# Kernel optimization log

Measured on AMD Instinct MI355X. Metric: run time of the kernel, lower is better.

## Reference

```python
import jax, jax.numpy as jnp
import numpy as np

N = 50000
IN_CH = 128
HID = 256
HEADS = 8
HEAD_DIM = HID // HEADS
NUM_CLASSES = 2
E = 800000
NEG_SLOPE = 0.2  # PyG GATConv default leaky_relu slope


def gat_conv(x, edge_index, W, att_src, att_dst, bias):
    """PyG-style GATConv (concat=True, add_self_loops=True, eval mode).
    x: [N, HID]; edge_index: [2, E] (row 0 = source j, row 1 = target i).
    W: [HID, HEADS*HEAD_DIM]; att_src/att_dst: [HEADS, HEAD_DIM]; bias: [HEADS*HEAD_DIM].
    """
    loop = jnp.arange(N)
    src = jnp.concatenate([edge_index[0], loop])  # self-loops appended
    dst = jnp.concatenate([edge_index[1], loop])
    h = (x @ W).reshape(N, HEADS, HEAD_DIM)          # [N, H, D]
    a_src = jnp.einsum('nhd,hd->nh', h, att_src)     # [N, H]
    a_dst = jnp.einsum('nhd,hd->nh', h, att_dst)
    e = jax.nn.leaky_relu(a_src[src] + a_dst[dst], NEG_SLOPE)  # [E+N, H]
    # segment softmax over incoming edges of each target node
    m = jax.ops.segment_max(e, dst, num_segments=N)
    p = jnp.exp(e - m[dst])
    s = jax.ops.segment_sum(p, dst, num_segments=N)
    alpha = p / (s[dst] + 1e-16)                     # [E+N, H]
    msg = h[src] * alpha[:, :, None]                 # [E+N, H, D]
    out = jax.ops.segment_sum(msg, dst, num_segments=N)  # [N, H, D]
    return out.reshape(N, HEADS * HEAD_DIM) + bias


def setup_inputs() -> dict:
    key = jax.random.key(0)
    ks = jax.random.split(key, 24)
    g = lambda k, shape, fan_in: jax.random.normal(k, shape, dtype=jnp.float32) / np.sqrt(fan_in)
    inp = {}
    inp['x'] = jax.random.normal(ks[0], (N, IN_CH), dtype=jnp.float32)
    inp['tut_edge_index'] = jax.random.randint(ks[1], (2, E), 0, N)
    inp['tdt_edge_index'] = jax.random.randint(ks[2], (2, E), 0, N)
    inp['proj_W'] = g(ks[3], (IN_CH, HID), IN_CH)
    inp['proj_b'] = jnp.zeros((HID,), jnp.float32)
    # 2 GAT layers per meta-path, stacked on leading axis
    inp['tut_W'] = g(ks[4], (2, HID, HID), HID)
    inp['tut_asrc'] = g(ks[5], (2, HEADS, HEAD_DIM), HEAD_DIM)
    inp['tut_adst'] = g(ks[6], (2, HEADS, HEAD_DIM), HEAD_DIM)
    inp['tut_bias'] = jnp.zeros((2, HID), jnp.float32)
    inp['tdt_W'] = g(ks[7], (2, HID, HID), HID)
    inp['tdt_asrc'] = g(ks[8], (2, HEADS, HEAD_DIM), HEAD_DIM)
    inp['tdt_adst'] = g(ks[9], (2, HEADS, HEAD_DIM), HEAD_DIM)
    inp['tdt_bias'] = jnp.zeros((2, HID), jnp.float32)
    inp['sem_att'] = jnp.full((2,), 0.5, jnp.float32)
    inp['cls_W1'] = g(ks[10], (HID, HID // 2), HID)
    inp['cls_b1'] = jnp.zeros((HID // 2,), jnp.float32)
    inp['cls_W2'] = g(ks[11], (HID // 2, NUM_CLASSES), HID // 2)
    inp['cls_b2'] = jnp.zeros((NUM_CLASSES,), jnp.float32)
    return inp


def reference(x, tut_edge_index, tdt_edge_index, proj_W, proj_b,
              tut_W, tut_asrc, tut_adst, tut_bias,
              tdt_W, tdt_asrc, tdt_adst, tdt_bias,
              sem_att, cls_W1, cls_b1, cls_W2, cls_b2):
    h = x @ proj_W + proj_b
    # TUT branch: 2 GATConv layers (eval mode -> dropout is identity)
    h_tut = h
    for l in range(2):
        h_tut = gat_conv(h_tut, tut_edge_index, tut_W[l], tut_asrc[l], tut_adst[l], tut_bias[l])
        h_tut = jax.nn.elu(h_tut)
    # TDT branch
    h_tdt = h
    for l in range(2):
        h_tdt = gat_conv(h_tdt, tdt_edge_index, tdt_W[l], tdt_asrc[l], tdt_adst[l], tdt_bias[l])
        h_tdt = jax.nn.elu(h_tdt)
    w = jax.nn.softmax(sem_att)
    z = w[0] * h_tut + w[1] * h_tdt
    hc = jax.nn.relu(z @ cls_W1 + cls_b1)
    logits = hc @ cls_W2 + cls_b2  # [N, NUM_CLASSES]
    return logits
```

## Files before the change

kernel.cpp:

```cpp
#include <hip/hip_runtime.h>
#include <hip/hip_fp16.h>
#include <cstddef>
#include <cstdint>


#define HID        256
#define HEADS      8
#define NEG_SLOPE  0.2f

#define BSH     7
#define BNODES  128
#define MAXNB   512
#define CH      2048

typedef __attribute__((ext_vector_type(8))) short short8v;
typedef __attribute__((ext_vector_type(4))) float float4v;

static __device__ __forceinline__ unsigned short f32_to_bf16(float v) {
    union { float f; unsigned u; } c; c.f = v;
    unsigned r = c.u + 0x7FFFu + ((c.u >> 16) & 1u);
    return (unsigned short)(r >> 16);
}
static __device__ __forceinline__ float bf16_to_f32(unsigned short b) {
    union { unsigned u; float f; } c; c.u = ((unsigned)b) << 16;
    return c.f;
}
static __device__ __forceinline__ void split_bf16(float v, unsigned short& hi, unsigned short& lo) {
    hi = f32_to_bf16(v);
    lo = f32_to_bf16(v - bf16_to_f32(hi));
}
static __device__ __forceinline__ void gload_lds16(const void* g, void* l) {
    __builtin_amdgcn_global_load_lds((const __attribute__((address_space(1))) void*)g,
                                     (__attribute__((address_space(3))) void*)l, 16, 0, 0);
}

template<int MODE>
__global__ __launch_bounds__(256) void mfma_gemm_kernel(
    const unsigned short* __restrict__ Ahi, const unsigned short* __restrict__ Alo,
    const unsigned short* __restrict__ Bthi, const unsigned short* __restrict__ Btlo,
    const float* __restrict__ bias,
    unsigned short* __restrict__ Chi, unsigned short* __restrict__ Clo,
    __half* __restrict__ Cf16, float* __restrict__ Cf32,
    int M, int N, int K)
{
    __shared__ __align__(16) short lds[4 * 4096];

    const int tid  = threadIdx.x;
    const int lane = tid & 63;
    const int w    = tid >> 6;
    const int wr   = w >> 1;
    const int wc   = w & 1;
    const int m0   = blockIdx.y * 128;
    const int n0   = blockIdx.x * 128;

    const unsigned short* sbase = (w == 0) ? Ahi : (w == 1) ? Alo : (w == 2) ? Bthi : Btlo;
    const int rowbase = (w < 2) ? m0 : n0;
    const int rowlim  = ((w < 2) ? M : N) - 1;

    float4v acc[4][4];
    #pragma unroll
    for (int i = 0; i < 4; ++i)
        #pragma unroll
        for (int j = 0; j < 4; ++j)
            acc[i][j] = (float4v){0.f, 0.f, 0.f, 0.f};

    const int kcl = lane >> 4;
    const int rl  = lane & 15;

    for (int k0 = 0; k0 < K; k0 += 32) {
        #pragma unroll
        for (int rh = 0; rh < 2; ++rh) {
            int row = rowbase + rh * 64 + lane;
            row = row > rowlim ? rowlim : row;
            const unsigned short* src = sbase + (size_t)row * K + k0;
            #pragma unroll
            for (int kc = 0; kc < 4; ++kc) {
                short* dst = &lds[w * 4096 + kc * 1024 + rh * 512];
                gload_lds16(src + kc * 8, dst);
            }
        }
        __syncthreads();

        short8v ahi[4], alo[4], bhi[4], blo[4];
        #pragma unroll
        for (int i = 0; i < 4; ++i) {
            int am = wr * 64 + i * 16 + rl;
            int bn = wc * 64 + i * 16 + rl;
            ahi[i] = *(const short8v*)&lds[0 * 4096 + kcl * 1024 + am * 8];
            alo[i] = *(const short8v*)&lds[1 * 4096 + kcl * 1024 + am * 8];
            bhi[i] = *(const short8v*)&lds[2 * 4096 + kcl * 1024 + bn * 8];
            blo[i] = *(const short8v*)&lds[3 * 4096 + kcl * 1024 + bn * 8];
        }
        #pragma unroll
        for (int i = 0; i < 4; ++i)
            #pragma unroll
            for (int j = 0; j < 4; ++j) {
                acc[i][j] = __builtin_amdgcn_mfma_f32_16x16x32_bf16(ahi[i], bhi[j], acc[i][j], 0, 0, 0);
                acc[i][j] = __builtin_amdgcn_mfma_f32_16x16x32_bf16(ahi[i], blo[j], acc[i][j], 0, 0, 0);
                acc[i][j] = __builtin_amdgcn_mfma_f32_16x16x32_bf16(alo[i], bhi[j], acc[i][j], 0, 0, 0);
            }
        __syncthreads();
    }

    const int cr = (lane >> 4) * 4;
    #pragma unroll
    for (int i = 0; i < 4; ++i) {
        #pragma unroll
        for (int r = 0; r < 4; ++r) {
            int row = m0 + wr * 64 + i * 16 + cr + r;
            if (row >= M) continue;
            #pragma unroll
            for (int j = 0; j < 4; ++j) {
                int col = n0 + wc * 64 + j * 16 + rl;
                float v = acc[i][j][r];
                if (bias) v += bias[col];
                if (MODE == 0) {
                    unsigned short h, l;
                    split_bf16(v, h, l);
                    Chi[(size_t)row * N + col] = h;
                    Clo[(size_t)row * N + col] = l;
                } else if (MODE == 1) {
                    Cf16[(size_t)row * N + col] = __float2half(v);
                } else {
                    Cf32[(size_t)row * N + col] = fmaxf(v, 0.f);
                }
            }
        }
    }
}

__global__ void prep_kernel(
    const float* __restrict__ proj_W, const float* __restrict__ tut_W,
    const float* __restrict__ tdt_W, const float* __restrict__ cls_W1,
    unsigned short* __restrict__ pWthi, unsigned short* __restrict__ pWtlo,
    unsigned short* __restrict__ tWthi, unsigned short* __restrict__ tWtlo,
    unsigned short* __restrict__ dWthi, unsigned short* __restrict__ dWtlo,
    unsigned short* __restrict__ cWthi, unsigned short* __restrict__ cWtlo,
    const float* __restrict__ x,
    unsigned short* __restrict__ xhi, unsigned short* __restrict__ xlo, int count4x)
{
    const int tid = blockIdx.x * blockDim.x + threadIdx.x;
    const int stride = gridDim.x * blockDim.x;
    for (int idx = tid; idx < 327680; idx += stride) {
        unsigned short h, l;
        if (idx < 32768) {
            int k = idx >> 8, n = idx & 255;
            split_bf16(proj_W[idx], h, l);
            pWthi[n * 128 + k] = h; pWtlo[n * 128 + k] = l;
        } else if (idx < 163840) {
            int r = idx - 32768;
            int ly = r >> 16, rr = r & 65535;
            int k = rr >> 8, n = rr & 255;
            split_bf16(tut_W[r], h, l);
            tWthi[ly * 65536 + n * 256 + k] = h; tWtlo[ly * 65536 + n * 256 + k] = l;
        } else if (idx < 294912) {
            int r = idx - 163840;
            int ly = r >> 16, rr = r & 65535;
            int k = rr >> 8, n = rr & 255;
            split_bf16(tdt_W[r], h, l);
            dWthi[ly * 65536 + n * 256 + k] = h; dWtlo[ly * 65536 + n * 256 + k] = l;
        } else {
            int r = idx - 294912;
            int k = r >> 7, n = r & 127;
            split_bf16(cls_W1[r], h, l);
            cWthi[n * 256 + k] = h; cWtlo[n * 256 + k] = l;
        }
    }
    for (int i = tid; i < count4x; i += stride) {
        float4 v = reinterpret_cast<const float4*>(x)[i];
        ushort4 hh, ll;
        split_bf16(v.x, hh.x, ll.x);
        split_bf16(v.y, hh.y, ll.y);
        split_bf16(v.z, hh.z, ll.z);
        split_bf16(v.w, hh.w, ll.w);
        reinterpret_cast<ushort4*>(xhi)[i] = hh;
        reinterpret_cast<ushort4*>(xlo)[i] = ll;
    }
}

__global__ __launch_bounds__(256) void att_kernel(
    const __half* __restrict__ hW,
    const float* __restrict__ att_src, const float* __restrict__ att_dst,
    float* __restrict__ a_src, float* __restrict__ a_dst, int n_nodes)
{
    const int wave = threadIdx.x >> 6;
    const int lane = threadIdx.x & 63;
    const int n = blockIdx.x * 4 + wave;
    if (n >= n_nodes) return;

    const __half2* hp = reinterpret_cast<const __half2*>(&hW[(size_t)n * HID + lane * 4]);
    __half2 h01 = hp[0], h23 = hp[1];
    float hx = __low2float(h01), hy = __high2float(h01);
    float hz = __low2float(h23), hw = __high2float(h23);
    float4 s4 = *reinterpret_cast<const float4*>(&att_src[lane * 4]);
    float4 d4 = *reinterpret_cast<const float4*>(&att_dst[lane * 4]);
    float ps = hx * s4.x + hy * s4.y + hz * s4.z + hw * s4.w;
    float pd = hx * d4.x + hy * d4.y + hz * d4.z + hw * d4.w;
    #pragma unroll
    for (int off = 1; off < 8; off <<= 1) {
        ps += __shfl_xor(ps, off);
        pd += __shfl_xor(pd, off);
    }
    if ((lane & 7) == 0) {
        a_src[n * HEADS + (lane >> 3)] = ps;
        a_dst[n * HEADS + (lane >> 3)] = pd;
    }
}

template<int OMODE>
__global__ __launch_bounds__(256) void gat_kernel(
    const __half* __restrict__ hW,
    const float* __restrict__ a_src, const float* __restrict__ a_dst,
    const int* __restrict__ row_ptr, const int* __restrict__ adj,
    const float* __restrict__ bias,
    const unsigned short* __restrict__ prevHi, const unsigned short* __restrict__ prevLo,
    const float* __restrict__ sem,
    unsigned short* __restrict__ outhi, unsigned short* __restrict__ outlo,
    int n_nodes)
{
    const int wave = threadIdx.x >> 6;
    const int lane = threadIdx.x & 63;
    const int n = blockIdx.x * 4 + wave;
    if (n >= n_nodes) return;

    const int beg = row_ptr[n];
    const int end = row_ptr[n + 1];
    const int h2 = lane >> 3;
    const int sl = lane & 7;
    const int lane4 = lane * 4;
    const int gbase = lane & 56;

    const float adst = a_dst[n * HEADS + h2];

    float m = -INFINITY, s = 0.f;
    float4 acc = make_float4(0.f, 0.f, 0.f, 0.f);

    for (int j = beg; j < end; j += 8) {
        const int js = j + sl;
        const int valid = js < end;
        int src_l = valid ? adj[js] : 0;
        float e = -INFINITY;
        if (valid) {
            e = a_src[src_l * HEADS + h2] + adst;
            e = (e > 0.f) ? e : NEG_SLOPE * e;
        }
        float me = e;
        me = fmaxf(me, __shfl_xor(me, 1));
        me = fmaxf(me, __shfl_xor(me, 2));
        me = fmaxf(me, __shfl_xor(me, 4));
        const float m_new = fmaxf(m, me);
        const float scale = __expf(m - m_new);
        const float p = __expf(e - m_new);
        float ps = p;
        ps += __shfl_xor(ps, 1);
        ps += __shfl_xor(ps, 2);
        ps += __shfl_xor(ps, 4);
        s = s * scale + ps;
        m = m_new;
        acc.x *= scale; acc.y *= scale; acc.z *= scale; acc.w *= scale;

        #pragma unroll
        for (int jj = 0; jj < 8; ++jj) {
            if (j + jj >= end) break;
            const float alpha = __shfl(p, gbase | jj);
            const int src = __shfl(src_l, jj);
            const __half2* hp = reinterpret_cast<const __half2*>(&hW[(size_t)src * HID + lane4]);
            __half2 v01 = hp[0], v23 = hp[1];
            acc.x += alpha * __low2float(v01);
            acc.y += alpha * __high2float(v01);
            acc.z += alpha * __low2float(v23);
            acc.w += alpha * __high2float(v23);
        }
    }

    const float inv = 1.f / (s + 1e-16f);
    float4 bv = *reinterpret_cast<const float4*>(&bias[lane4]);
    float4 o;
    o.x = acc.x * inv + bv.x; o.y = acc.y * inv + bv.y;
    o.z = acc.z * inv + bv.z; o.w = acc.w * inv + bv.w;
    o.x = (o.x > 0.f) ? o.x : expm1f(o.x);
    o.y = (o.y > 0.f) ? o.y : expm1f(o.y);
    o.z = (o.z > 0.f) ? o.z : expm1f(o.z);
    o.w = (o.w > 0.f) ? o.w : expm1f(o.w);

    if (OMODE == 1) {
        const float e0 = __expf(sem[0]);
        const float e1 = __expf(sem[1]);
        const float w0 = e0 / (e0 + e1);
        const float w1 = e1 / (e0 + e1);
        ushort4 ph = *reinterpret_cast<const ushort4*>(&prevHi[(size_t)n * HID + lane4]);
        ushort4 pl = *reinterpret_cast<const ushort4*>(&prevLo[(size_t)n * HID + lane4]);
        o.x = w0 * (bf16_to_f32(ph.x) + bf16_to_f32(pl.x)) + w1 * o.x;
        o.y = w0 * (bf16_to_f32(ph.y) + bf16_to_f32(pl.y)) + w1 * o.y;
        o.z = w0 * (bf16_to_f32(ph.z) + bf16_to_f32(pl.z)) + w1 * o.z;
        o.w = w0 * (bf16_to_f32(ph.w) + bf16_to_f32(pl.w)) + w1 * o.w;
    }

    ushort4 oh, ol;
    split_bf16(o.x, oh.x, ol.x);
    split_bf16(o.y, oh.y, ol.y);
    split_bf16(o.z, oh.z, ol.z);
    split_bf16(o.w, oh.w, ol.w);
    *reinterpret_cast<ushort4*>(&outhi[(size_t)n * HID + lane4]) = oh;
    *reinterpret_cast<ushort4*>(&outlo[(size_t)n * HID + lane4]) = ol;
}

__global__ __launch_bounds__(256) void bucket_count_kernel(
    const int* __restrict__ tut_dst, const int* __restrict__ tdt_dst,
    int* __restrict__ gcount, int E, int NB)
{
    __shared__ int hist[MAXNB];
    const int g = blockIdx.y;
    const int* dstp = g ? tdt_dst : tut_dst;
    for (int i = threadIdx.x; i < MAXNB; i += 256) hist[i] = 0;
    __syncthreads();
    for (int e = blockIdx.x * 256 + threadIdx.x; e < E; e += gridDim.x * 256)
        atomicAdd(&hist[dstp[e] >> BSH], 1);
    __syncthreads();
    for (int i = threadIdx.x; i < NB; i += 256) {
        int c = hist[i];
        if (c) atomicAdd(&gcount[g * NB + i], c);
    }
}

__global__ __launch_bounds__(512) void bucket_scan_kernel(
    const int* __restrict__ gcount, int* __restrict__ ebase, int* __restrict__ adjbase,
    int* __restrict__ rp0, int* __restrict__ rp1, int N, int E, int NB)
{
    __shared__ int sa[MAXNB], sb[MAXNB];
    const int t = threadIdx.x;
    for (int g = 0; g < 2; ++g) {
        int cnt = (t < NB) ? gcount[g * NB + t] : 0;
        int nodes = 0;
        if (t < NB) { int s = t << BSH; nodes = (N - s < BNODES) ? (N - s) : BNODES; }
        sa[t] = cnt;
        sb[t] = cnt + nodes;
        __syncthreads();
        for (int off = 1; off < MAXNB; off <<= 1) {
            int va = (t >= off) ? sa[t - off] : 0;
            int vb = (t >= off) ? sb[t - off] : 0;
            __syncthreads();
            sa[t] += va; sb[t] += vb;
            __syncthreads();
        }
        if (t < NB) {
            ebase[g * (NB + 1) + t + 1] = sa[t];
            adjbase[g * (NB + 1) + t + 1] = sb[t];
        }
        if (t == 0) { ebase[g * (NB + 1)] = 0; adjbase[g * (NB + 1)] = 0; }
        __syncthreads();
    }
    if (t == 0) { rp0[N] = E + N; rp1[N] = E + N; }
}

__global__ __launch_bounds__(256) void bucket_bin_kernel(
    const int* __restrict__ tut_ei, const int* __restrict__ tdt_ei,
    const int* __restrict__ ebase, int* __restrict__ gcursor,
    int2* __restrict__ ebuf, int E, int NB)
{
    __shared__ int lhist[MAXNB];
    __shared__ int lbase[MAXNB];
    __shared__ int loffs[MAXNB];
    __shared__ int2 spair[CH];
    __shared__ int saddr[CH];
    const int g = blockIdx.y;
    const int* ei = g ? tdt_ei : tut_ei;
    const int e0 = blockIdx.x * CH;
    const int cnt = (E - e0 < CH) ? (E - e0) : CH;

    for (int i = threadIdx.x; i < MAXNB; i += 256) lhist[i] = 0;
    __syncthreads();

    int myb[8], myrank[8], mysrc[8], mydst[8];
    int nmine = 0;
    #pragma unroll
    for (int k = 0; k < 8; ++k) {
        int idx = e0 + threadIdx.x + k * 256;
        if (idx < e0 + cnt) {
            int sv = ei[idx];
            int dv = ei[E + idx];
            int b = dv >> BSH;
            int r = atomicAdd(&lhist[b], 1);
            myb[nmine] = b; myrank[nmine] = r; mysrc[nmine] = sv; mydst[nmine] = dv;
            ++nmine;
        }
    }
    __syncthreads();
    loffs[threadIdx.x] = lhist[threadIdx.x];
    loffs[threadIdx.x + 256] = lhist[threadIdx.x + 256];
    __syncthreads();
    for (int off = 1; off < MAXNB; off <<= 1) {
        int i0 = threadIdx.x, i1 = threadIdx.x + 256;
        int v0 = (i0 >= off) ? loffs[i0 - off] : 0;
        int v1 = (i1 >= off) ? loffs[i1 - off] : 0;
        __syncthreads();
        loffs[i0] += v0; loffs[i1] += v1;
        __syncthreads();
    }
    for (int i = threadIdx.x; i < NB; i += 256) {
        int c = lhist[i];
        lbase[i] = c ? atomicAdd(&gcursor[g * NB + i], c) : 0;
    }
    __syncthreads();
    const int* eb = ebase + g * (NB + 1);
    for (int k = 0; k < nmine; ++k) {
        int b = myb[k];
        int sorted = loffs[b] - lhist[b] + myrank[k];
        spair[sorted] = make_int2(mysrc[k], mydst[k]);
        saddr[sorted] = eb[b] + lbase[b] + myrank[k];
    }
    __syncthreads();
    int2* out = ebuf + (size_t)g * E;
    for (int i = threadIdx.x; i < cnt; i += 256)
        out[saddr[i]] = spair[i];
}

__global__ __launch_bounds__(256) void bucket_csr_kernel(
    const int* __restrict__ gcount, const int* __restrict__ ebase,
    const int* __restrict__ adjbase, const int2* __restrict__ ebuf,
    int* __restrict__ rp0, int* __restrict__ rp1,
    int* __restrict__ adj0, int* __restrict__ adj1, int N, int E, int NB)
{
    __shared__ int hist[BNODES], scn[BNODES], cursor[BNODES];
    const int g = blockIdx.y;
    const int b = blockIdx.x;
    int* rp  = g ? rp1 : rp0;
    int* adj = g ? adj1 : adj0;
    const int cnt = gcount[g * NB + b];
    const int aB  = adjbase[g * (NB + 1) + b];
    const int node0 = b << BSH;
    const int nb = (N - node0 < BNODES) ? (N - node0) : BNODES;
    const int2* ep = ebuf + (size_t)g * E + ebase[g * (NB + 1) + b];
    const int t = threadIdx.x;

    if (t < BNODES) hist[t] = 0;
    __syncthreads();
    for (int e = t; e < cnt; e += 256)
        atomicAdd(&hist[ep[e].y - node0], 1);
    __syncthreads();
    if (t < BNODES) scn[t] = (t < nb) ? hist[t] + 1 : 0;
    __syncthreads();
    for (int off = 1; off < BNODES; off <<= 1) {
        int v = 0;
        if (t < BNODES && t >= off) v = scn[t - off];
        __syncthreads();
        if (t < BNODES) scn[t] += v;
        __syncthreads();
    }
    if (t < nb) {
        int s = scn[t] - hist[t] - 1;
        rp[node0 + t] = aB + s;
        adj[aB + s] = node0 + t;
        cursor[t] = s + 1;
    }
    __syncthreads();
    for (int e = t; e < cnt; e += 256) {
        int2 pr = ep[e];
        int pos = atomicAdd(&cursor[pr.y - node0], 1);
        adj[aB + pos] = pr.x;
    }
}

__global__ __launch_bounds__(256) void cls2_kernel(
    const float* __restrict__ hc, const float* __restrict__ W2,
    const float* __restrict__ b2, float* __restrict__ out, int n_nodes)
{
    const int wave = threadIdx.x >> 6;
    const int lane = threadIdx.x & 63;
    const int n = blockIdx.x * 4 + wave;
    if (n >= n_nodes) return;
    float h0 = hc[(size_t)n * 128 + lane];
    float h1 = hc[(size_t)n * 128 + 64 + lane];
    float p0 = h0 * W2[lane * 2 + 0] + h1 * W2[(64 + lane) * 2 + 0];
    float p1 = h0 * W2[lane * 2 + 1] + h1 * W2[(64 + lane) * 2 + 1];
    #pragma unroll
    for (int off = 1; off < 64; off <<= 1) {
        p0 += __shfl_xor(p0, off);
        p1 += __shfl_xor(p1, off);
    }
    if (lane == 0) {
        out[(size_t)n * 2 + 0] = p0 + b2[0];
        out[(size_t)n * 2 + 1] = p1 + b2[1];
    }
}

extern "C" void kernel_launch(void* const* d_in, const int* in_sizes, int n_in,
                              void* d_out, int out_size, void* d_ws, size_t ws_size,
                              hipStream_t stream)
{
    const float* x        = (const float*)d_in[0];
    const int*   tut_ei   = (const int*)d_in[1];
    const int*   tdt_ei   = (const int*)d_in[2];
    const float* proj_W   = (const float*)d_in[3];
    const float* proj_b   = (const float*)d_in[4];
    const float* tut_W    = (const float*)d_in[5];
    const float* tut_asrc = (const float*)d_in[6];
    const float* tut_adst = (const float*)d_in[7];
    const float* tut_bias = (const float*)d_in[8];
    const float* tdt_W    = (const float*)d_in[9];
    const float* tdt_asrc = (const float*)d_in[10];
    const float* tdt_adst = (const float*)d_in[11];
    const float* tdt_bias = (const float*)d_in[12];
    const float* sem_att  = (const float*)d_in[13];
    const float* cls_W1   = (const float*)d_in[14];
    const float* cls_b1   = (const float*)d_in[15];
    const float* cls_W2   = (const float*)d_in[16];
    const float* cls_b2   = (const float*)d_in[17];

    const int IN_CH = 128;
    const int N = in_sizes[0] / IN_CH;
    const int E = in_sizes[1] / 2;
    const int NB = (N + BNODES - 1) >> BSH;
    const size_t NH = (size_t)N * HID;
    const size_t NI = (size_t)N * IN_CH;

    char* base = (char*)d_ws;
    size_t off = 0;
    auto alloc = [&](size_t bytes) -> void* {
        void* p = base + off;
        off = (off + bytes + 255) & ~(size_t)255;
        return p;
    };
    unsigned short* xhi  = (unsigned short*)alloc(NI * 2);
    unsigned short* xlo  = (unsigned short*)alloc(NI * 2);
    unsigned short* t2lo = (unsigned short*)alloc(NH * 2);
    unsigned short* h0hi = (unsigned short*)alloc(NH * 2);
    unsigned short* h0lo = (unsigned short*)alloc(NH * 2);
    unsigned short* l1hi = (unsigned short*)alloc(NH * 2);
    unsigned short* l1lo = (unsigned short*)alloc(NH * 2);
    __half*         hWf  = (__half*)alloc(NH * 2);
    float* a_src = (float*)alloc((size_t)N * HEADS * sizeof(float));
    float* a_dst = (float*)alloc((size_t)N * HEADS * sizeof(float));
    unsigned short* pWthi = (unsigned short*)alloc(256 * 128 * 2);
    unsigned short* pWtlo = (unsigned short*)alloc(256 * 128 * 2);
    unsigned short* tWthi = (unsigned short*)alloc(2 * 256 * 256 * 2);
    unsigned short* tWtlo = (unsigned short*)alloc(2 * 256 * 256 * 2);
    unsigned short* dWthi = (unsigned short*)alloc(2 * 256 * 256 * 2);
    unsigned short* dWtlo = (unsigned short*)alloc(2 * 256 * 256 * 2);
    unsigned short* cWthi = (unsigned short*)alloc(128 * 256 * 2);
    unsigned short* cWtlo = (unsigned short*)alloc(128 * 256 * 2);
    int* rp_tut  = (int*)alloc((size_t)(N + 1) * sizeof(int));
    int* adj_tut = (int*)alloc((size_t)(E + N) * sizeof(int));
    int* rp_tdt  = (int*)alloc((size_t)(N + 1) * sizeof(int));
    int* adj_tdt = (int*)alloc((size_t)(E + N) * sizeof(int));
    int* gbuf    = (int*)alloc((size_t)4 * NB * sizeof(int));
    int* gcount  = gbuf;
    int* gcursor = gbuf + 2 * NB;
    int* ebase   = (int*)alloc((size_t)2 * (NB + 1) * sizeof(int));
    int* adjbase = (int*)alloc((size_t)2 * (NB + 1) * sizeof(int));
    (void)ws_size; (void)n_in; (void)out_size;

    int2* ebuf = (int2*)hWf;
    unsigned short* t2hi = xhi;
    unsigned short* zhi  = l1hi;
    unsigned short* zlo  = l1lo;
    float*          hc   = (float*)hWf;

    const int nodeBlocks = (N + 3) / 4;

    hipMemsetAsync(gbuf, 0, (size_t)4 * NB * sizeof(int), stream);
    prep_kernel<<<1024, 256, 0, stream>>>(proj_W, tut_W, tdt_W, cls_W1,
                                          pWthi, pWtlo, tWthi, tWtlo, dWthi, dWtlo,
                                          cWthi, cWtlo, x, xhi, xlo, (int)(NI / 4));
    bucket_count_kernel<<<dim3(128, 2), 256, 0, stream>>>(tut_ei + E, tdt_ei + E, gcount, E, NB);
    bucket_scan_kernel<<<1, 512, 0, stream>>>(gcount, ebase, adjbase, rp_tut, rp_tdt, N, E, NB);
    bucket_bin_kernel<<<dim3((E + CH - 1) / CH, 2), 256, 0, stream>>>(
        tut_ei, tdt_ei, ebase, gcursor, ebuf, E, NB);
    bucket_csr_kernel<<<dim3(NB, 2), 256, 0, stream>>>(
        gcount, ebase, adjbase, ebuf, rp_tut, rp_tdt, adj_tut, adj_tdt, N, E, NB);

    const int gy = (N + 127) / 128;

    mfma_gemm_kernel<0><<<dim3(2, gy), 256, 0, stream>>>(
        xhi, xlo, pWthi, pWtlo, proj_b, h0hi, h0lo, nullptr, nullptr, N, HID, IN_CH);

    auto run_gemm_att = [&](const unsigned short* ahi, const unsigned short* alo,
                            const unsigned short* wthi, const unsigned short* wtlo,
                            const float* asrc_w, const float* adst_w) {
        mfma_gemm_kernel<1><<<dim3(2, gy), 256, 0, stream>>>(
            ahi, alo, wthi, wtlo, nullptr, nullptr, nullptr, hWf, nullptr, N, HID, HID);
        att_kernel<<<nodeBlocks, 256, 0, stream>>>(hWf, asrc_w, adst_w, a_src, a_dst, N);
    };

    const int WT = 256 * 256;
    const int AS = HEADS * (HID / HEADS);

    run_gemm_att(h0hi, h0lo, tWthi, tWtlo, tut_asrc, tut_adst);
    gat_kernel<0><<<nodeBlocks, 256, 0, stream>>>(
        hWf, a_src, a_dst, rp_tut, adj_tut, tut_bias,
        nullptr, nullptr, nullptr, l1hi, l1lo, N);
    run_gemm_att(l1hi, l1lo, tWthi + WT, tWtlo + WT, tut_asrc + AS, tut_adst + AS);
    gat_kernel<0><<<nodeBlocks, 256, 0, stream>>>(
        hWf, a_src, a_dst, rp_tut, adj_tut, tut_bias + HID,
        nullptr, nullptr, nullptr, t2hi, t2lo, N);
    run_gemm_att(h0hi, h0lo, dWthi, dWtlo, tdt_asrc, tdt_adst);
    gat_kernel<0><<<nodeBlocks, 256, 0, stream>>>(
        hWf, a_src, a_dst, rp_tdt, adj_tdt, tdt_bias,
        nullptr, nullptr, nullptr, l1hi, l1lo, N);
    run_gemm_att(l1hi, l1lo, dWthi + WT, dWtlo + WT, tdt_asrc + AS, tdt_adst + AS);
    gat_kernel<1><<<nodeBlocks, 256, 0, stream>>>(
        hWf, a_src, a_dst, rp_tdt, adj_tdt, tdt_bias + HID,
        t2hi, t2lo, sem_att, zhi, zlo, N);

    mfma_gemm_kernel<2><<<dim3(1, gy), 256, 0, stream>>>(
        zhi, zlo, cWthi, cWtlo, cls_b1, nullptr, nullptr, nullptr, hc, N, 128, HID);
    cls2_kernel<<<nodeBlocks, 256, 0, stream>>>(hc, cls_W2, cls_b2, (float*)d_out, N);
}
```

Before: 759.3 us.

## Fuse first-layer GEMMs of both branches, two-pass GAT softmax, pack edge pairs

Merges the first GAT layer projection of the TUT and TDT branches into a single 512-wide GEMM sharing the h0 input, writing two separate fp16 outputs. Rewrites the GAT aggregation as a two-pass scheme: first a per-head max/sum reduction across lanes, then an unrolled gather loop with precomputed normalized alphas, which removes the per-chunk rescaling and shuffles. Packs source and local destination into one int in the CSR build to halve edge buffer traffic. The two-pass approach reads adj and a_src twice, and the buffer aliasing is more involved.

```diff
diff --git a/kernel.cpp b/kernel.cpp
--- a/kernel.cpp
+++ b/kernel.cpp
@@ -40,7 +40,7 @@
     const unsigned short* __restrict__ Bthi, const unsigned short* __restrict__ Btlo,
     const float* __restrict__ bias,
     unsigned short* __restrict__ Chi, unsigned short* __restrict__ Clo,
-    __half* __restrict__ Cf16, float* __restrict__ Cf32,
+    __half* __restrict__ Cf16a, __half* __restrict__ Cf16b, float* __restrict__ Cf32,
     int M, int N, int K)
 {
     __shared__ __align__(16) short lds[4 * 4096];
@@ -120,7 +120,8 @@
                     Chi[(size_t)row * N + col] = h;
                     Clo[(size_t)row * N + col] = l;
                 } else if (MODE == 1) {
-                    Cf16[(size_t)row * N + col] = __float2half(v);
+                    if (col < 256) Cf16a[(size_t)row * 256 + col] = __float2half(v);
+                    else           Cf16b[(size_t)row * 256 + (col - 256)] = __float2half(v);
                 } else {
                     Cf32[(size_t)row * N + col] = fmaxf(v, 0.f);
                 }
@@ -133,8 +134,9 @@
     const float* __restrict__ proj_W, const float* __restrict__ tut_W,
     const float* __restrict__ tdt_W, const float* __restrict__ cls_W1,
     unsigned short* __restrict__ pWthi, unsigned short* __restrict__ pWtlo,
-    unsigned short* __restrict__ tWthi, unsigned short* __restrict__ tWtlo,
-    unsigned short* __restrict__ dWthi, unsigned short* __restrict__ dWtlo,
+    unsigned short* __restrict__ w1hi,  unsigned short* __restrict__ w1lo,
+    unsigned short* __restrict__ t2Whi, unsigned short* __restrict__ t2Wlo,
+    unsigned short* __restrict__ d2Whi, unsigned short* __restrict__ d2Wlo,
     unsigned short* __restrict__ cWthi, unsigned short* __restrict__ cWtlo,
     const float* __restrict__ x,
     unsigned short* __restrict__ xhi, unsigned short* __restrict__ xlo, int count4x)
@@ -152,13 +154,15 @@
             int ly = r >> 16, rr = r & 65535;
             int k = rr >> 8, n = rr & 255;
             split_bf16(tut_W[r], h, l);
-            tWthi[ly * 65536 + n * 256 + k] = h; tWtlo[ly * 65536 + n * 256 + k] = l;
+            if (ly == 0) { w1hi[n * 256 + k] = h;  w1lo[n * 256 + k] = l; }
+            else         { t2Whi[n * 256 + k] = h; t2Wlo[n * 256 + k] = l; }
         } else if (idx < 294912) {
             int r = idx - 163840;
             int ly = r >> 16, rr = r & 65535;
             int k = rr >> 8, n = rr & 255;
             split_bf16(tdt_W[r], h, l);
-            dWthi[ly * 65536 + n * 256 + k] = h; dWtlo[ly * 65536 + n * 256 + k] = l;
+            if (ly == 0) { w1hi[(256 + n) * 256 + k] = h; w1lo[(256 + n) * 256 + k] = l; }
+            else         { d2Whi[n * 256 + k] = h;        d2Wlo[n * 256 + k] = l; }
         } else {
             int r = idx - 294912;
             int k = r >> 7, n = r & 127;
@@ -225,59 +229,83 @@
 
     const int beg = row_ptr[n];
     const int end = row_ptr[n + 1];
+    const int h1 = lane & 7;
+    const float adst1 = a_dst[n * HEADS + h1];
+
+    float m = -INFINITY, s = 0.f;
+    for (int j = beg + (lane >> 3); j < end; j += 8) {
+        float e = a_src[adj[j] * HEADS + h1] + adst1;
+        e = (e > 0.f) ? e : NEG_SLOPE * e;
+        float mn = fmaxf(m, e);
+        float t = (m > -INFINITY) ? s * __expf(m - mn) : 0.f;
+        s = t + __expf(e - mn);
+        m = mn;
+    }
+    #pragma unroll
+    for (int off = 8; off < 64; off <<= 1) {
+        float mo = __shfl_xor(m, off);
+        float so = __shfl_xor(s, off);
+        float mn = fmaxf(m, mo);
+        float t1 = (m  > -INFINITY) ? s  * __expf(m  - mn) : 0.f;
+        float t2 = (mo > -INFINITY) ? so * __expf(mo - mn) : 0.f;
+        s = t1 + t2;
+        m = mn;
+    }
+
     const int h2 = lane >> 3;
-    const int sl = lane & 7;
+    const float mh  = __shfl(m, h2);
+    const float sh  = __shfl(s, h2);
+    const float inv = 1.f / (sh + 1e-16f);
+    const float adst2 = a_dst[n * HEADS + h2];
     const int lane4 = lane * 4;
-    const int gbase = lane & 56;
-
-    const float adst = a_dst[n * HEADS + h2];
-
-    float m = -INFINITY, s = 0.f;
+
     float4 acc = make_float4(0.f, 0.f, 0.f, 0.f);
-
-    for (int j = beg; j < end; j += 8) {
-        const int js = j + sl;
-        const int valid = js < end;
-        int src_l = valid ? adj[js] : 0;
-        float e = -INFINITY;
-        if (valid) {
-            e = a_src[src_l * HEADS + h2] + adst;
-            e = (e > 0.f) ? e : NEG_SLOPE * e;
-        }
-        float me = e;
-        me = fmaxf(me, __shfl_xor(me, 1));
-        me = fmaxf(me, __shfl_xor(me, 2));
-        me = fmaxf(me, __shfl_xor(me, 4));
-        const float m_new = fmaxf(m, me);
-        const float scale = __expf(m - m_new);
-        const float p = __expf(e - m_new);
-        float ps = p;
-        ps += __shfl_xor(ps, 1);
-        ps += __shfl_xor(ps, 2);
-        ps += __shfl_xor(ps, 4);
-        s = s * scale + ps;
-        m = m_new;
-        acc.x *= scale; acc.y *= scale; acc.z *= scale; acc.w *= scale;
-
-        #pragma unroll
-        for (int jj = 0; jj < 8; ++jj) {
-            if (j + jj >= end) break;
-            const float alpha = __shfl(p, gbase | jj);
-            const int src = __shfl(src_l, jj);
-            const __half2* hp = reinterpret_cast<const __half2*>(&hW[(size_t)src * HID + lane4]);
-            __half2 v01 = hp[0], v23 = hp[1];
-            acc.x += alpha * __low2float(v01);
-            acc.y += alpha * __high2float(v01);
-            acc.z += alpha * __low2float(v23);
-            acc.w += alpha * __high2float(v23);
-        }
-    }
-
-    const float inv = 1.f / (s + 1e-16f);
+    int j = beg;
+    for (; j + 4 <= end; j += 4) {
+        int s0 = adj[j + 0], s1 = adj[j + 1], s2 = adj[j + 2], s3 = adj[j + 3];
+        float e0 = a_src[s0 * HEADS + h2] + adst2;
+        float e1 = a_src[s1 * HEADS + h2] + adst2;
+        float e2 = a_src[s2 * HEADS + h2] + adst2;
+        float e3 = a_src[s3 * HEADS + h2] + adst2;
+        e0 = (e0 > 0.f) ? e0 : NEG_SLOPE * e0;
+        e1 = (e1 > 0.f) ? e1 : NEG_SLOPE * e1;
+        e2 = (e2 > 0.f) ? e2 : NEG_SLOPE * e2;
+        e3 = (e3 > 0.f) ? e3 : NEG_SLOPE * e3;
+        float al0 = __expf(e0 - mh) * inv;
+        float al1 = __expf(e1 - mh) * inv;
+        float al2 = __expf(e2 - mh) * inv;
+        float al3 = __expf(e3 - mh) * inv;
+        const __half2* p0 = reinterpret_cast<const __half2*>(&hW[(size_t)s0 * HID + lane4]);
+        const __half2* p1 = reinterpret_cast<const __half2*>(&hW[(size_t)s1 * HID + lane4]);
+        const __half2* p2 = reinterpret_cast<const __half2*>(&hW[(size_t)s2 * HID + lane4]);
+        const __half2* p3 = reinterpret_cast<const __half2*>(&hW[(size_t)s3 * HID + lane4]);
+        __half2 a01 = p0[0], a23 = p0[1];
+        __half2 b01 = p1[0], b23 = p1[1];
+        __half2 c01 = p2[0], c23 = p2[1];
+        __half2 d01 = p3[0], d23 = p3[1];
+        acc.x += al0 * __low2float(a01); acc.y += al0 * __high2float(a01);
+        acc.z += al0 * __low2float(a23); acc.w += al0 * __high2float(a23);
+        acc.x += al1 * __low2float(b01); acc.y += al1 * __high2float(b01);
+        acc.z += al1 * __low2float(b23); acc.w += al1 * __high2float(b23);
+        acc.x += al2 * __low2float(c01); acc.y += al2 * __high2float(c01);
+        acc.z += al2 * __low2float(c23); acc.w += al2 * __high2float(c23);
+        acc.x += al3 * __low2float(d01); acc.y += al3 * __high2float(d01);
+        acc.z += al3 * __low2float(d23); acc.w += al3 * __high2float(d23);
+    }
+    for (; j < end; ++j) {
+        int src = adj[j];
+        float e = a_src[src * HEADS + h2] + adst2;
+        e = (e > 0.f) ? e : NEG_SLOPE * e;
+        float alpha = __expf(e - mh) * inv;
+        const __half2* p = reinterpret_cast<const __half2*>(&hW[(size_t)src * HID + lane4]);
+        __half2 a01 = p[0], a23 = p[1];
+        acc.x += alpha * __low2float(a01); acc.y += alpha * __high2float(a01);
+        acc.z += alpha * __low2float(a23); acc.w += alpha * __high2float(a23);
+    }
+
     float4 bv = *reinterpret_cast<const float4*>(&bias[lane4]);
     float4 o;
-    o.x = acc.x * inv + bv.x; o.y = acc.y * inv + bv.y;
-    o.z = acc.z * inv + bv.z; o.w = acc.w * inv + bv.w;
+    o.x = acc.x + bv.x; o.y = acc.y + bv.y; o.z = acc.z + bv.z; o.w = acc.w + bv.w;
     o.x = (o.x > 0.f) ? o.x : expm1f(o.x);
     o.y = (o.y > 0.f) ? o.y : expm1f(o.y);
     o.z = (o.z > 0.f) ? o.z : expm1f(o.z);
@@ -356,12 +384,12 @@
 __global__ __launch_bounds__(256) void bucket_bin_kernel(
     const int* __restrict__ tut_ei, const int* __restrict__ tdt_ei,
     const int* __restrict__ ebase, int* __restrict__ gcursor,
-    int2* __restrict__ ebuf, int E, int NB)
+    int* __restrict__ ebuf, int E, int NB)
 {
     __shared__ int lhist[MAXNB];
     __shared__ int lbase[MAXNB];
     __shared__ int loffs[MAXNB];
-    __shared__ int2 spair[CH];
+    __shared__ int spair[CH];
     __shared__ int saddr[CH];
     const int g = blockIdx.y;
     const int* ei = g ? tdt_ei : tut_ei;
@@ -371,7 +399,7 @@
     for (int i = threadIdx.x; i < MAXNB; i += 256) lhist[i] = 0;
     __syncthreads();
 
-    int myb[8], myrank[8], mysrc[8], mydst[8];
+    int myb[8], myrank[8], mypk[8];
     int nmine = 0;
     #pragma unroll
     for (int k = 0; k < 8; ++k) {
@@ -381,7 +409,8 @@
             int dv = ei[E + idx];
             int b = dv >> BSH;
             int r = atomicAdd(&lhist[b], 1);
-            myb[nmine] = b; myrank[nmine] = r; mysrc[nmine] = sv; mydst[nmine] = dv;
+            myb[nmine] = b; myrank[nmine] = r;
+            mypk[nmine] = (sv << BSH) | (dv & (BNODES - 1));
             ++nmine;
         }
     }
@@ -406,18 +435,18 @@
     for (int k = 0; k < nmine; ++k) {
         int b = myb[k];
         int sorted = loffs[b] - lhist[b] + myrank[k];
-        spair[sorted] = make_int2(mysrc[k], mydst[k]);
+        spair[sorted] = mypk[k];
         saddr[sorted] = eb[b] + lbase[b] + myrank[k];
     }
     __syncthreads();
-    int2* out = ebuf + (size_t)g * E;
+    int* out = ebuf + (size_t)g * E;
     for (int i = threadIdx.x; i < cnt; i += 256)
         out[saddr[i]] = spair[i];
 }
 
 __global__ __launch_bounds__(256) void bucket_csr_kernel(
     const int* __restrict__ gcount, const int* __restrict__ ebase,
-    const int* __restrict__ adjbase, const int2* __restrict__ ebuf,
+    const int* __restrict__ adjbase, const int* __restrict__ ebuf,
     int* __restrict__ rp0, int* __restrict__ rp1,
     int* __restrict__ adj0, int* __restrict__ adj1, int N, int E, int NB)
 {
@@ -430,13 +459,13 @@
     const int aB  = adjbase[g * (NB + 1) + b];
     const int node0 = b << BSH;
     const int nb = (N - node0 < BNODES) ? (N - node0) : BNODES;
-    const int2* ep = ebuf + (size_t)g * E + ebase[g * (NB + 1) + b];
+    const int* ep = ebuf + (size_t)g * E + ebase[g * (NB + 1) + b];
     const int t = threadIdx.x;
 
     if (t < BNODES) hist[t] = 0;
     __syncthreads();
     for (int e = t; e < cnt; e += 256)
-        atomicAdd(&hist[ep[e].y - node0], 1);
+        atomicAdd(&hist[ep[e] & (BNODES - 1)], 1);
     __syncthreads();
     if (t < BNODES) scn[t] = (t < nb) ? hist[t] + 1 : 0;
     __syncthreads();
@@ -455,9 +484,9 @@
     }
     __syncthreads();
     for (int e = t; e < cnt; e += 256) {
-        int2 pr = ep[e];
-        int pos = atomicAdd(&cursor[pr.y - node0], 1);
-        adj[aB + pos] = pr.x;
+        int p = ep[e];
+        int pos = atomicAdd(&cursor[p & (BNODES - 1)], 1);
+        adj[aB + pos] = p >> BSH;
     }
 }
 
@@ -521,22 +550,26 @@
         off = (off + bytes + 255) & ~(size_t)255;
         return p;
     };
-    unsigned short* xhi  = (unsigned short*)alloc(NI * 2);
-    unsigned short* xlo  = (unsigned short*)alloc(NI * 2);
-    unsigned short* t2lo = (unsigned short*)alloc(NH * 2);
-    unsigned short* h0hi = (unsigned short*)alloc(NH * 2);
-    unsigned short* h0lo = (unsigned short*)alloc(NH * 2);
-    unsigned short* l1hi = (unsigned short*)alloc(NH * 2);
-    unsigned short* l1lo = (unsigned short*)alloc(NH * 2);
-    __half*         hWf  = (__half*)alloc(NH * 2);
-    float* a_src = (float*)alloc((size_t)N * HEADS * sizeof(float));
-    float* a_dst = (float*)alloc((size_t)N * HEADS * sizeof(float));
+    unsigned short* xhi   = (unsigned short*)alloc(NI * 2);
+    unsigned short* xlo   = (unsigned short*)alloc(NI * 2);
+    unsigned short* t2lo  = (unsigned short*)alloc(NH * 2);
+    unsigned short* h0hi  = (unsigned short*)alloc(NH * 2);
+    unsigned short* h0lo  = (unsigned short*)alloc(NH * 2);
+    unsigned short* l1thi = (unsigned short*)alloc(NH * 2);
+    unsigned short* l1tlo = (unsigned short*)alloc(NH * 2);
+    __half*         hWa   = (__half*)alloc(NH * 2);
+    float* as1 = (float*)alloc((size_t)N * HEADS * sizeof(float));
+    float* ad1 = (float*)alloc((size_t)N * HEADS * sizeof(float));
+    float* as2 = (float*)alloc((size_t)N * HEADS * sizeof(float));
+    float* ad2 = (float*)alloc((size_t)N * HEADS * sizeof(float));
     unsigned short* pWthi = (unsigned short*)alloc(256 * 128 * 2);
     unsigned short* pWtlo = (unsigned short*)alloc(256 * 128 * 2);
-    unsigned short* tWthi = (unsigned short*)alloc(2 * 256 * 256 * 2);
-    unsigned short* tWtlo = (unsigned short*)alloc(2 * 256 * 256 * 2);
-    unsigned short* dWthi = (unsigned short*)alloc(2 * 256 * 256 * 2);
-    unsigned short* dWtlo = (unsigned short*)alloc(2 * 256 * 256 * 2);
+    unsigned short* w1hi  = (unsigned short*)alloc(512 * 256 * 2);
+    unsigned short* w1lo  = (unsigned short*)alloc(512 * 256 * 2);
+    unsigned short* t2Whi = (unsigned short*)alloc(256 * 256 * 2);
+    unsigned short* t2Wlo = (unsigned short*)alloc(256 * 256 * 2);
+    unsigned short* d2Whi = (unsigned short*)alloc(256 * 256 * 2);
+    unsigned short* d2Wlo = (unsigned short*)alloc(256 * 256 * 2);
     unsigned short* cWthi = (unsigned short*)alloc(128 * 256 * 2);
     unsigned short* cWtlo = (unsigned short*)alloc(128 * 256 * 2);
     int* rp_tut  = (int*)alloc((size_t)(N + 1) * sizeof(int));
@@ -550,18 +583,22 @@
     int* adjbase = (int*)alloc((size_t)2 * (NB + 1) * sizeof(int));
     (void)ws_size; (void)n_in; (void)out_size;
 
-    int2* ebuf = (int2*)hWf;
+    int* ebuf = (int*)hWa;
+    __half* hWb = (__half*)t2lo;
     unsigned short* t2hi = xhi;
-    unsigned short* zhi  = l1hi;
-    unsigned short* zlo  = l1lo;
-    float*          hc   = (float*)hWf;
+    unsigned short* l1dhi = h0hi;
+    unsigned short* l1dlo = h0lo;
+    unsigned short* zhi = l1thi;
+    unsigned short* zlo = l1tlo;
+    float* hc = (float*)hWa;
 
     const int nodeBlocks = (N + 3) / 4;
 
     hipMemsetAsync(gbuf, 0, (size_t)4 * NB * sizeof(int), stream);
     prep_kernel<<<1024, 256, 0, stream>>>(proj_W, tut_W, tdt_W, cls_W1,
-                                          pWthi, pWtlo, tWthi, tWtlo, dWthi, dWtlo,
-                                          cWthi, cWtlo, x, xhi, xlo, (int)(NI / 4));
+                                          pWthi, pWtlo, w1hi, w1lo, t2Whi, t2Wlo,
+                                          d2Whi, d2Wlo, cWthi, cWtlo,
+                                          x, xhi, xlo, (int)(NI / 4));
     bucket_count_kernel<<<dim3(128, 2), 256, 0, stream>>>(tut_ei + E, tdt_ei + E, gcount, E, NB);
     bucket_scan_kernel<<<1, 512, 0, stream>>>(gcount, ebase, adjbase, rp_tut, rp_tdt, N, E, NB);
     bucket_bin_kernel<<<dim3((E + CH - 1) / CH, 2), 256, 0, stream>>>(
@@ -570,39 +607,42 @@
         gcount, ebase, adjbase, ebuf, rp_tut, rp_tdt, adj_tut, adj_tdt, N, E, NB);
 
     const int gy = (N + 127) / 128;
+    const int AS = HEADS * (HID / HEADS);
 
     mfma_gemm_kernel<0><<<dim3(2, gy), 256, 0, stream>>>(
-        xhi, xlo, pWthi, pWtlo, proj_b, h0hi, h0lo, nullptr, nullptr, N, HID, IN_CH);
-
-    auto run_gemm_att = [&](const unsigned short* ahi, const unsigned short* alo,
-                            const unsigned short* wthi, const unsigned short* wtlo,
-                            const float* asrc_w, const float* adst_w) {
-        mfma_gemm_kernel<1><<<dim3(2, gy), 256, 0, stream>>>(
-            ahi, alo, wthi, wtlo, nullptr, nullptr, nullptr, hWf, nullptr, N, HID, HID);
-        att_kernel<<<nodeBlocks, 256, 0, stream>>>(hWf, asrc_w, adst_w, a_src, a_dst, N);
-    };
-
-    const int WT = 256 * 256;
-    const int AS = HEADS * (HID / HEADS);
-
-    run_gemm_att(h0hi, h0lo, tWthi, tWtlo, tut_asrc, tut_adst);
+        xhi, xlo, pWthi, pWtlo, proj_b, h0hi, h0lo, nullptr, nullptr, nullptr,
+        N, HID, IN_CH);
+
+    mfma_gemm_kernel<1><<<dim3(4, gy), 256, 0, stream>>>(
+        h0hi, h0lo, w1hi, w1lo, nullptr, nullptr, nullptr, hWa, hWb, nullptr,
+        N, 512, HID);
+    att_kernel<<<nodeBlocks, 256, 0, stream>>>(hWa, tut_asrc, tut_adst, as1, ad1, N);
+    att_kernel<<<nodeBlocks, 256, 0, stream>>>(hWb, tdt_asrc, tdt_adst, as2, ad2, N);
     gat_kernel<0><<<nodeBlocks, 256, 0, stream>>>(
-        hWf, a_src, a_dst, rp_tut, adj_tut, tut_bias,
-        nullptr, nullptr, nullptr, l1hi, l1lo, N);
-    run_gemm_att(l1hi, l1lo, tWthi + WT, tWtlo + WT, tut_asrc + AS, tut_adst + AS);
+        hWa, as1, ad1, rp_tut, adj_tut, tut_bias,
+        nullptr, nullptr, nullptr, l1thi, l1tlo, N);
     gat_kernel<0><<<nodeBlocks, 256, 0, stream>>>(
-        hWf, a_src, a_dst, rp_tut, adj_tut, tut_bias + HID,
+        hWb, as2, ad2, rp_tdt, adj_tdt, tdt_bias,
+        nullptr, nullptr, nullptr, l1dhi, l1dlo, N);
+
+    mfma_gemm_kernel<1><<<dim3(2, gy), 256, 0, stream>>>(
+        l1thi, l1tlo, t2Whi, t2Wlo, nullptr, nullptr, nullptr, hWa, nullptr, nullptr,
+        N, HID, HID);
+    att_kernel<<<nodeBlocks, 256, 0, stream>>>(hWa, tut_asrc + AS, tut_adst + AS, as1, ad1, N);
+    gat_kernel<0><<<nodeBlocks, 256, 0, stream>>>(
+        hWa, as1, ad1, rp_tut, adj_tut, tut_bias + HID,
         nullptr, nullptr, nullptr, t2hi, t2lo, N);
-    run_gemm_att(h0hi, h0lo, dWthi, dWtlo, tdt_asrc, tdt_adst);
-    gat_kernel<0><<<nodeBlocks, 256, 0, stream>>>(
-        hWf, a_src, a_dst, rp_tdt, adj_tdt, tdt_bias,
-        nullptr, nullptr, nullptr, l1hi, l1lo, N);
-    run_gemm_att(l1hi, l1lo, dWthi + WT, dWtlo + WT, tdt_asrc + AS, tdt_adst + AS);
+
+    mfma_gemm_kernel<1><<<dim3(2, gy), 256, 0, stream>>>(
+        l1dhi, l1dlo, d2Whi, d2Wlo, nullptr, nullptr, nullptr, hWa, nullptr, nullptr,
+        N, HID, HID);
+    att_kernel<<<nodeBlocks, 256, 0, stream>>>(hWa, tdt_asrc + AS, tdt_adst + AS, as2, ad2, N);
     gat_kernel<1><<<nodeBlocks, 256, 0, stream>>>(
-        hWf, a_src, a_dst, rp_tdt, adj_tdt, tdt_bias + HID,
+        hWa, as2, ad2, rp_tdt, adj_tdt, tdt_bias + HID,
         t2hi, t2lo, sem_att, zhi, zlo, N);
 
     mfma_gemm_kernel<2><<<dim3(1, gy), 256, 0, stream>>>(
-        zhi, zlo, cWthi, cWtlo, cls_b1, nullptr, nullptr, nullptr, hc, N, 128, HID);
+        zhi, zlo, cWthi, cWtlo, cls_b1, nullptr, nullptr, nullptr, nullptr, hc,
+        N, 128, HID);
     cls2_kernel<<<nodeBlocks, 256, 0, stream>>>(hc, cls_W2, cls_b2, (float*)d_out, N);
 }
```

Measured after the change: 728.7 us. -4.0%, faster.
